# Performance work log

Hardware: AMD Instinct MI355X
Metric: run time of the kernel (lower is better)

The kernel has to match this reference:

```python
import jax, jax.numpy as jnp
import numpy as np

N = 100_000   # total nodes (batched graph)
E = 1_600_000 # edges (avg degree 16)
W = 100       # window_size (node feature dim)
H = 60        # hidden = ceil(0.6 * window_size)


def setup_inputs() -> dict:
    key = jax.random.key(0)
    ks = jax.random.split(key, 6)
    x = jax.random.normal(ks[0], (N, W), dtype=jnp.float32)
    batch_edge_index = jax.random.randint(ks[1], (2, E), 0, N, dtype=jnp.int32)
    gcn_w = jax.random.normal(ks[2], (W, W), dtype=jnp.float32) * 0.1
    gcn_b = jnp.zeros((W,), dtype=jnp.float32)
    w1 = jax.random.normal(ks[3], (H, W), dtype=jnp.float32) * 0.1
    b1 = jnp.zeros((H,), dtype=jnp.float32)
    w2 = jax.random.normal(ks[4], (W, H), dtype=jnp.float32) * 0.1
    b2 = jnp.zeros((W,), dtype=jnp.float32)
    return {"x": x, "batch_edge_index": batch_edge_index,
            "gcn_w": gcn_w, "gcn_b": gcn_b,
            "w1": w1, "b1": b1, "w2": w2, "b2": b2}


def reference(x, batch_edge_index, gcn_w, gcn_b, w1, b1, w2, b2):
    n = x.shape[0]
    # GCNConv: add self-loops, symmetric normalization D^-1/2 A D^-1/2
    loop = jnp.arange(n, dtype=batch_edge_index.dtype)
    src = jnp.concatenate([batch_edge_index[0], loop])
    dst = jnp.concatenate([batch_edge_index[1], loop])
    deg = jax.ops.segment_sum(jnp.ones(src.shape[0], jnp.float32), dst, num_segments=n)
    dinv = jnp.where(deg > 0, jax.lax.rsqrt(deg), 0.0)
    norm = dinv[src] * dinv[dst]                      # [E+N]
    xw = x @ gcn_w.T                                  # [N, W] linear transform
    msg = xw[src] * norm[:, None]                     # gather + scale
    out = jax.ops.segment_sum(msg, dst, num_segments=n) + gcn_b  # scatter-add
    # relu + tanh MLP head
    h = jax.nn.relu(out)
    h = jnp.tanh(h @ w1.T + b1)
    return jnp.tanh(h @ w2.T + b2)
```

## Files before the change

kernel.cpp:

```cpp
#include <hip/hip_runtime.h>
#include <hip/hip_bf16.h>

#define WDIM 100
#define HDIM 60
#define NPART 8
#define CAP 64

typedef short bf16x8 __attribute__((ext_vector_type(8)));
typedef float f32x4 __attribute__((ext_vector_type(4)));

__device__ inline unsigned short bf_hi_u(float v) {
    return __bfloat16_as_ushort(__float2bfloat16(v));
}
__device__ inline unsigned int pack2(float v0, float v1) {
    return (unsigned int)bf_hi_u(v0) | ((unsigned int)bf_hi_u(v1) << 16);
}
__device__ inline float fast_tanh(float x) {
    float xc = fminf(fmaxf(x, -15.f), 15.f);
    float t = __expf(2.f * xc);
    return __fdividef(t - 1.f, t + 1.f);
}

__global__ __launch_bounds__(256) void k_zero(int* __restrict__ cnt, int N) {
    int i = blockIdx.x * blockDim.x + threadIdx.x;
    int stride = gridDim.x * blockDim.x;
    for (int idx = i; idx < N; idx += stride) cnt[idx] = 0;
}

__global__ __launch_bounds__(256) void k_fill(const int* __restrict__ src,
                                              const int* __restrict__ dst,
                                              int* __restrict__ cursor,
                                              int* __restrict__ e_idx, int E, int npp) {
    const int xcd = blockIdx.x & (NPART - 1);
    const int lo = xcd * npp, hi = lo + npp;
    const int4* __restrict__ dst4 = (const int4*)dst;
    const int4* __restrict__ src4 = (const int4*)src;
    int E4 = E >> 2;
    int i = (blockIdx.x >> 3) * blockDim.x + threadIdx.x;
    int stride = (gridDim.x >> 3) * blockDim.x;
    for (int e = i; e < E4; e += stride) {
        int4 d = dst4[e];
        int4 s = src4[e];
        if (d.x >= lo && d.x < hi) {
            int p = atomicAdd(&cursor[d.x], 1);
            if (p < CAP) e_idx[(size_t)d.x * CAP + p] = s.x;
        }
        if (d.y >= lo && d.y < hi) {
            int p = atomicAdd(&cursor[d.y], 1);
            if (p < CAP) e_idx[(size_t)d.y * CAP + p] = s.y;
        }
        if (d.z >= lo && d.z < hi) {
            int p = atomicAdd(&cursor[d.z], 1);
            if (p < CAP) e_idx[(size_t)d.z * CAP + p] = s.z;
        }
        if (d.w >= lo && d.w < hi) {
            int p = atomicAdd(&cursor[d.w], 1);
            if (p < CAP) e_idx[(size_t)d.w * CAP + p] = s.w;
        }
    }
    if (i == 0) {
        for (int e = E4 << 2; e < E; ++e) {
            int d = dst[e];
            if (d >= lo && d < hi) {
                int p = atomicAdd(&cursor[d], 1);
                if (p < CAP) e_idx[(size_t)d * CAP + p] = src[e];
            }
        }
    }
}

__global__ __launch_bounds__(256) void k_xw(const float* __restrict__ x,
                                            const float* __restrict__ gw,
                                            const int* __restrict__ cnt,
                                            unsigned int* __restrict__ xwh,
                                            int N, int ntiles) {
    __shared__ char wlds[112 * 256];
    const int tid = threadIdx.x;
    for (int w = tid; w < 112 * 64; w += 256) {
        int j = w >> 6, kp = w & 63;
        unsigned int val = 0;
        if (j < 100 && kp < 50)
            val = pack2(gw[j * 100 + 2 * kp], gw[j * 100 + 2 * kp + 1]);
        *(unsigned int*)&wlds[j * 256 + ((kp * 4) ^ ((j & 7) << 4))] = val;
    }
    __syncthreads();

    const int wv = tid >> 6, l = tid & 63;
    const int arow = wv * 16 + (l & 15);
    const int koff = (l >> 4) * 8;
    const int cl = l & 15;
    const int nodeb = wv * 16 + (l >> 4) * 4;

    for (int tile = blockIdx.x; tile < ntiles; tile += gridDim.x) {
        const int n0 = tile * 64;
        int ga = n0 + arow;
        int grow = (ga < N) ? ga : (N - 1);
        const float* __restrict__ xr = x + (size_t)grow * 100;
        bf16x8 ah[4];
#pragma unroll
        for (int kt = 0; kt < 4; ++kt) {
            int c0 = kt * 32 + koff;
            float4 fa = (c0 + 4 <= 100) ? *(const float4*)&xr[c0]
                                        : make_float4(0.f, 0.f, 0.f, 0.f);
            float4 fb = (c0 + 8 <= 100) ? *(const float4*)&xr[c0 + 4]
                                        : make_float4(0.f, 0.f, 0.f, 0.f);
            union { unsigned int u[4]; bf16x8 v; } uu;
            uu.u[0] = pack2(fa.x, fa.y);
            uu.u[1] = pack2(fa.z, fa.w);
            uu.u[2] = pack2(fb.x, fb.y);
            uu.u[3] = pack2(fb.z, fb.w);
            ah[kt] = uu.v;
        }
        float dir[4];
#pragma unroll
        for (int r = 0; r < 4; ++r) {
            int g = n0 + nodeb + r;
            dir[r] = (g < N) ? rsqrtf((float)(cnt[g] + 1)) : 0.0f;
        }
#pragma unroll
        for (int jt = 0; jt < 7; ++jt) {
            f32x4 acc = {0.f, 0.f, 0.f, 0.f};
#pragma unroll
            for (int kt = 0; kt < 4; ++kt) {
                int brow = jt * 16 + cl;
                int off = brow * 256 + (((kt * 32 + koff) * 2) ^ ((brow & 7) << 4));
                bf16x8 b = *(const bf16x8*)&wlds[off];
                acc = __builtin_amdgcn_mfma_f32_16x16x32_bf16(ah[kt], b, acc, 0, 0, 0);
            }
            int col = jt * 16 + cl;
#pragma unroll
            for (int r = 0; r < 4; ++r) {
                int g = n0 + nodeb + r;
                float v = acc[r] * dir[r];
                float o = __shfl_xor(v, 1);
                if (!(cl & 1) && col < 100 && g < N)
                    xwh[(size_t)g * 50 + (col >> 1)] = pack2(v, o);
            }
        }
    }
}

__global__ __launch_bounds__(256) void k_gather(const int* __restrict__ e_idx,
                                                const int* __restrict__ cnt,
                                                const unsigned int* __restrict__ xwh,
                                                const float* __restrict__ gb,
                                                unsigned int* __restrict__ acch, int N) {
    int wid = (blockIdx.x * blockDim.x + threadIdx.x) >> 6;
    int lane = threadIdx.x & 63;
    if (wid >= N) return;
    int lanec = (lane < 50) ? lane : 0;
    const int* __restrict__ row = e_idx + (size_t)wid * CAP;
    int numraw = cnt[wid];
    int num = (numraw < CAP) ? numraw : CAP;
    float di = rsqrtf((float)(numraw + 1));
    float a0 = 0.f, a1 = 0.f, b0 = 0.f, b1 = 0.f;
    float c0 = 0.f, c1 = 0.f, d0 = 0.f, d1 = 0.f;
    float e0 = 0.f, e1 = 0.f, f0 = 0.f, f1 = 0.f;
    float g0 = 0.f, g1 = 0.f, h0 = 0.f, h1 = 0.f;
    int k = 0;
    int nn8 = num & ~7;
    if (nn8) {
        unsigned int u0 = xwh[(size_t)row[0] * 50 + lanec];
        unsigned int u1 = xwh[(size_t)row[1] * 50 + lanec];
        unsigned int u2 = xwh[(size_t)row[2] * 50 + lanec];
        unsigned int u3 = xwh[(size_t)row[3] * 50 + lanec];
        unsigned int u4 = xwh[(size_t)row[4] * 50 + lanec];
        unsigned int u5 = xwh[(size_t)row[5] * 50 + lanec];
        unsigned int u6 = xwh[(size_t)row[6] * 50 + lanec];
        unsigned int u7 = xwh[(size_t)row[7] * 50 + lanec];
        for (k = 8; k < nn8; k += 8) {
            unsigned int v0 = xwh[(size_t)row[k + 0] * 50 + lanec];
            unsigned int v1 = xwh[(size_t)row[k + 1] * 50 + lanec];
            unsigned int v2 = xwh[(size_t)row[k + 2] * 50 + lanec];
            unsigned int v3 = xwh[(size_t)row[k + 3] * 50 + lanec];
            unsigned int v4 = xwh[(size_t)row[k + 4] * 50 + lanec];
            unsigned int v5 = xwh[(size_t)row[k + 5] * 50 + lanec];
            unsigned int v6 = xwh[(size_t)row[k + 6] * 50 + lanec];
            unsigned int v7 = xwh[(size_t)row[k + 7] * 50 + lanec];
            a0 += __uint_as_float(u0 << 16); a1 += __uint_as_float(u0 & 0xffff0000u);
            b0 += __uint_as_float(u1 << 16); b1 += __uint_as_float(u1 & 0xffff0000u);
            c0 += __uint_as_float(u2 << 16); c1 += __uint_as_float(u2 & 0xffff0000u);
            d0 += __uint_as_float(u3 << 16); d1 += __uint_as_float(u3 & 0xffff0000u);
            e0 += __uint_as_float(u4 << 16); e1 += __uint_as_float(u4 & 0xffff0000u);
            f0 += __uint_as_float(u5 << 16); f1 += __uint_as_float(u5 & 0xffff0000u);
            g0 += __uint_as_float(u6 << 16); g1 += __uint_as_float(u6 & 0xffff0000u);
            h0 += __uint_as_float(u7 << 16); h1 += __uint_as_float(u7 & 0xffff0000u);
            u0 = v0; u1 = v1; u2 = v2; u3 = v3;
            u4 = v4; u5 = v5; u6 = v6; u7 = v7;
        }
        a0 += __uint_as_float(u0 << 16); a1 += __uint_as_float(u0 & 0xffff0000u);
        b0 += __uint_as_float(u1 << 16); b1 += __uint_as_float(u1 & 0xffff0000u);
        c0 += __uint_as_float(u2 << 16); c1 += __uint_as_float(u2 & 0xffff0000u);
        d0 += __uint_as_float(u3 << 16); d1 += __uint_as_float(u3 & 0xffff0000u);
        e0 += __uint_as_float(u4 << 16); e1 += __uint_as_float(u4 & 0xffff0000u);
        f0 += __uint_as_float(u5 << 16); f1 += __uint_as_float(u5 & 0xffff0000u);
        g0 += __uint_as_float(u6 << 16); g1 += __uint_as_float(u6 & 0xffff0000u);
        h0 += __uint_as_float(u7 << 16); h1 += __uint_as_float(u7 & 0xffff0000u);
        k = nn8;
    }
    for (; k < num; ++k) {
        unsigned int u = xwh[(size_t)row[k] * 50 + lanec];
        a0 += __uint_as_float(u << 16); a1 += __uint_as_float(u & 0xffff0000u);
    }
    unsigned int us = xwh[(size_t)wid * 50 + lanec];
    float s0 = ((a0 + b0) + (c0 + d0)) + ((e0 + f0) + (g0 + h0)) + __uint_as_float(us << 16);
    float s1 = ((a1 + b1) + (c1 + d1)) + ((e1 + f1) + (g1 + h1)) + __uint_as_float(us & 0xffff0000u);
    if (lane < 50) {
        float2 gbv = *(const float2*)(gb + 2 * lane);
        float v0 = fmaxf(fmaf(s0, di, gbv.x), 0.0f);
        float v1 = fmaxf(fmaf(s1, di, gbv.y), 0.0f);
        acch[(size_t)wid * 50 + lane] = pack2(v0, v1);
    }
}

__global__ __launch_bounds__(256) void k_hout(const unsigned int* __restrict__ acch,
                                              const float* __restrict__ w1,
                                              const float* __restrict__ b1,
                                              const float* __restrict__ w2,
                                              const float* __restrict__ b2,
                                              float* __restrict__ out,
                                              int N, int ntiles) {
    __shared__ char w1lds[64 * 256];
    __shared__ char w2lds[112 * 128];
    __shared__ char hlds[64 * 128];
    const int tid = threadIdx.x;

    for (int w = tid; w < 64 * 64; w += 256) {
        int j = w >> 6, kp = w & 63;
        unsigned int val = 0;
        if (j < 60 && kp < 50)
            val = pack2(w1[j * 100 + 2 * kp], w1[j * 100 + 2 * kp + 1]);
        *(unsigned int*)&w1lds[j * 256 + ((kp * 4) ^ ((j & 7) << 4))] = val;
    }
    for (int w = tid; w < 112 * 32; w += 256) {
        int j = w >> 5, kp = w & 31;
        unsigned int val = 0;
        if (j < 100 && kp < 30)
            val = pack2(w2[j * 60 + 2 * kp], w2[j * 60 + 2 * kp + 1]);
        *(unsigned int*)&w2lds[j * 128 + ((kp * 4) ^ ((j & 7) << 4))] = val;
    }
    __syncthreads();

    const int wv = tid >> 6, l = tid & 63;
    const int arow = wv * 16 + (l & 15);
    const int koff = (l >> 4) * 8;
    const int cl = l & 15;
    const int nodeb = wv * 16 + (l >> 4) * 4;

    for (int tile = blockIdx.x; tile < ntiles; tile += gridDim.x) {
        const int n0 = tile * 64;
        int ga = n0 + arow;
        int grow = (ga < N) ? ga : (N - 1);
        const unsigned int* __restrict__ ar = acch + (size_t)grow * 50;
        bf16x8 ah2[4];
#pragma unroll
        for (int kt = 0; kt < 4; ++kt) {
            int c0 = kt * 32 + koff;
            int w0 = c0 >> 1;
            uint4 u = make_uint4(0u, 0u, 0u, 0u);
            if (c0 + 8 <= 100) {
                u = *(const uint4*)&ar[w0];
            } else if (c0 + 4 <= 100) {
                uint2 t = *(const uint2*)&ar[w0];
                u.x = t.x; u.y = t.y;
            }
            union { uint4 q; bf16x8 v; } uu; uu.q = u;
            ah2[kt] = uu.v;
        }
        __syncthreads();

#pragma unroll
        for (int jt = 0; jt < 4; ++jt) {
            f32x4 acc = {0.f, 0.f, 0.f, 0.f};
#pragma unroll
            for (int kt = 0; kt < 4; ++kt) {
                int brow = jt * 16 + cl;
                int off = brow * 256 + (((kt * 32 + koff) * 2) ^ ((brow & 7) << 4));
                bf16x8 b = *(const bf16x8*)&w1lds[off];
                acc = __builtin_amdgcn_mfma_f32_16x16x32_bf16(ah2[kt], b, acc, 0, 0, 0);
            }
            int col = jt * 16 + cl;
            float bias = (col < 60) ? b1[col] : 0.0f;
#pragma unroll
            for (int r = 0; r < 4; ++r) {
                float hv = (col < 60) ? fast_tanh(acc[r] + bias) : 0.0f;
                int node = nodeb + r;
                *(unsigned short*)&hlds[node * 128 + ((col * 2) ^ ((node & 7) << 4))] = bf_hi_u(hv);
            }
        }
        __syncthreads();

        bf16x8 ah3[2];
#pragma unroll
        for (int kt = 0; kt < 2; ++kt) {
            int off = arow * 128 + (((kt * 32 + koff) * 2) ^ ((arow & 7) << 4));
            ah3[kt] = *(const bf16x8*)&hlds[off];
        }

#pragma unroll
        for (int jt = 0; jt < 7; ++jt) {
            f32x4 acc = {0.f, 0.f, 0.f, 0.f};
#pragma unroll
            for (int kt = 0; kt < 2; ++kt) {
                int brow = jt * 16 + cl;
                int off = brow * 128 + (((kt * 32 + koff) * 2) ^ ((brow & 7) << 4));
                bf16x8 b = *(const bf16x8*)&w2lds[off];
                acc = __builtin_amdgcn_mfma_f32_16x16x32_bf16(ah3[kt], b, acc, 0, 0, 0);
            }
            int col = jt * 16 + cl;
            float bias = (col < 100) ? b2[col] : 0.0f;
#pragma unroll
            for (int r = 0; r < 4; ++r) {
                int g = n0 + nodeb + r;
                if (g < N && col < 100)
                    out[(size_t)g * 100 + col] = fast_tanh(acc[r] + bias);
            }
        }
    }
}

extern "C" void kernel_launch(void* const* d_in, const int* in_sizes, int n_in,
                              void* d_out, int out_size, void* d_ws, size_t ws_size,
                              hipStream_t stream) {
    const float* x   = (const float*)d_in[0];
    const int*   ei  = (const int*)d_in[1];
    const float* gw  = (const float*)d_in[2];
    const float* gb  = (const float*)d_in[3];
    const float* w1  = (const float*)d_in[4];
    const float* b1  = (const float*)d_in[5];
    const float* w2  = (const float*)d_in[6];
    const float* b2  = (const float*)d_in[7];
    float* out = (float*)d_out;

    const int W = in_sizes[3];
    const int N = in_sizes[0] / W;
    const int E = in_sizes[1] / 2;

    const int* src = ei;
    const int* dst = ei + E;

    unsigned int* xwh  = (unsigned int*)d_ws;
    unsigned int* acch = xwh + (size_t)N * 50;
    int*   e_idx = (int*)(acch + (size_t)N * 50);
    int*   cursor = e_idx + (size_t)N * CAP;

    const int B = 256;
    const int NT = (N + 63) / 64;
    const int npp = (N + NPART - 1) / NPART;
    auto blocks = [](long long work, int cap) {
        long long b = (work + 255) / 256;
        return (int)(b < cap ? b : cap);
    };

    k_zero<<<blocks(N, 2048), B, 0, stream>>>(cursor, N);
    k_fill<<<8192, B, 0, stream>>>(src, dst, cursor, e_idx, E, npp);
    k_xw<<<782, B, 0, stream>>>(x, gw, cursor, xwh, N, NT);
    k_gather<<<(N * 64 + B - 1) / B, B, 0, stream>>>(e_idx, cursor, xwh, gb, acch, N);
    k_hout<<<782, B, 0, stream>>>(acch, w1, b1, w2, b2, out, N, NT);
}
```

Baseline: 222.3 us.

## Fuse edge fill and XW GEMM into one launch, move source scaling to gather

Combines the CSR-style edge bucketing kernel and the x@W^T MFMA kernel into one launch: the first 4096 blocks do the atomic fill and the rest compute XW, so the two independent stages can run concurrently. To remove XW's dependence on degree counts, the source-side D^-1/2 scaling moves from XW into the gather, which now loads cnt for each neighbor and applies rsqrt per edge. This adds one extra random 4-byte load and rsqrt per edge in the gather. The fill grid also drops from 8192 to 4096 blocks.

```diff
diff --git a/kernel.cpp b/kernel.cpp
--- a/kernel.cpp
+++ b/kernel.cpp
@@ -5,6 +5,7 @@
 #define HDIM 60
 #define NPART 8
 #define CAP 64
+#define FILLB 4096
 
 typedef short bf16x8 __attribute__((ext_vector_type(8)));
 typedef float f32x4 __attribute__((ext_vector_type(4)));
@@ -27,55 +28,59 @@
     for (int idx = i; idx < N; idx += stride) cnt[idx] = 0;
 }
 
-__global__ __launch_bounds__(256) void k_fill(const int* __restrict__ src,
-                                              const int* __restrict__ dst,
-                                              int* __restrict__ cursor,
-                                              int* __restrict__ e_idx, int E, int npp) {
-    const int xcd = blockIdx.x & (NPART - 1);
-    const int lo = xcd * npp, hi = lo + npp;
-    const int4* __restrict__ dst4 = (const int4*)dst;
-    const int4* __restrict__ src4 = (const int4*)src;
-    int E4 = E >> 2;
-    int i = (blockIdx.x >> 3) * blockDim.x + threadIdx.x;
-    int stride = (gridDim.x >> 3) * blockDim.x;
-    for (int e = i; e < E4; e += stride) {
-        int4 d = dst4[e];
-        int4 s = src4[e];
-        if (d.x >= lo && d.x < hi) {
-            int p = atomicAdd(&cursor[d.x], 1);
-            if (p < CAP) e_idx[(size_t)d.x * CAP + p] = s.x;
-        }
-        if (d.y >= lo && d.y < hi) {
-            int p = atomicAdd(&cursor[d.y], 1);
-            if (p < CAP) e_idx[(size_t)d.y * CAP + p] = s.y;
-        }
-        if (d.z >= lo && d.z < hi) {
-            int p = atomicAdd(&cursor[d.z], 1);
-            if (p < CAP) e_idx[(size_t)d.z * CAP + p] = s.z;
-        }
-        if (d.w >= lo && d.w < hi) {
-            int p = atomicAdd(&cursor[d.w], 1);
-            if (p < CAP) e_idx[(size_t)d.w * CAP + p] = s.w;
-        }
-    }
-    if (i == 0) {
-        for (int e = E4 << 2; e < E; ++e) {
-            int d = dst[e];
-            if (d >= lo && d < hi) {
-                int p = atomicAdd(&cursor[d], 1);
-                if (p < CAP) e_idx[(size_t)d * CAP + p] = src[e];
-            }
-        }
-    }
-}
-
-__global__ __launch_bounds__(256) void k_xw(const float* __restrict__ x,
-                                            const float* __restrict__ gw,
-                                            const int* __restrict__ cnt,
-                                            unsigned int* __restrict__ xwh,
-                                            int N, int ntiles) {
+__global__ __launch_bounds__(256) void k_fillxw(const int* __restrict__ src,
+                                                const int* __restrict__ dst,
+                                                int* __restrict__ cursor,
+                                                int* __restrict__ e_idx,
+                                                int E, int npp,
+                                                const float* __restrict__ x,
+                                                const float* __restrict__ gw,
+                                                unsigned int* __restrict__ xwh,
+                                                int N, int ntiles) {
     __shared__ char wlds[112 * 256];
     const int tid = threadIdx.x;
+    const int b = blockIdx.x;
+
+    if (b < FILLB) {
+        const int xcd = b & (NPART - 1);
+        const int lo = xcd * npp, hi = lo + npp;
+        const int4* __restrict__ dst4 = (const int4*)dst;
+        const int4* __restrict__ src4 = (const int4*)src;
+        int E4 = E >> 2;
+        int i = (b >> 3) * 256 + tid;
+        int stride = (FILLB >> 3) * 256;
+        for (int e = i; e < E4; e += stride) {
+            int4 d = dst4[e];
+            int4 s = src4[e];
+            if (d.x >= lo && d.x < hi) {
+                int p = atomicAdd(&cursor[d.x], 1);
+                if (p < CAP) e_idx[(size_t)d.x * CAP + p] = s.x;
+            }
+            if (d.y >= lo && d.y < hi) {
+                int p = atomicAdd(&cursor[d.y], 1);
+                if (p < CAP) e_idx[(size_t)d.y * CAP + p] = s.y;
+            }
+            if (d.z >= lo && d.z < hi) {
+                int p = atomicAdd(&cursor[d.z], 1);
+                if (p < CAP) e_idx[(size_t)d.z * CAP + p] = s.z;
+            }
+            if (d.w >= lo && d.w < hi) {
+                int p = atomicAdd(&cursor[d.w], 1);
+                if (p < CAP) e_idx[(size_t)d.w * CAP + p] = s.w;
+            }
+        }
+        if (i == 0) {
+            for (int e = E4 << 2; e < E; ++e) {
+                int d = dst[e];
+                if (d >= lo && d < hi) {
+                    int p = atomicAdd(&cursor[d], 1);
+                    if (p < CAP) e_idx[(size_t)d * CAP + p] = src[e];
+                }
+            }
+        }
+        return;
+    }
+
     for (int w = tid; w < 112 * 64; w += 256) {
         int j = w >> 6, kp = w & 63;
         unsigned int val = 0;
@@ -90,8 +95,9 @@
     const int koff = (l >> 4) * 8;
     const int cl = l & 15;
     const int nodeb = wv * 16 + (l >> 4) * 4;
-
-    for (int tile = blockIdx.x; tile < ntiles; tile += gridDim.x) {
+    const int xwb = gridDim.x - FILLB;
+
+    for (int tile = b - FILLB; tile < ntiles; tile += xwb) {
         const int n0 = tile * 64;
         int ga = n0 + arow;
         int grow = (ga < N) ? ga : (N - 1);
@@ -111,12 +117,6 @@
             uu.u[3] = pack2(fb.z, fb.w);
             ah[kt] = uu.v;
         }
-        float dir[4];
-#pragma unroll
-        for (int r = 0; r < 4; ++r) {
-            int g = n0 + nodeb + r;
-            dir[r] = (g < N) ? rsqrtf((float)(cnt[g] + 1)) : 0.0f;
-        }
 #pragma unroll
         for (int jt = 0; jt < 7; ++jt) {
             f32x4 acc = {0.f, 0.f, 0.f, 0.f};
@@ -124,14 +124,14 @@
             for (int kt = 0; kt < 4; ++kt) {
                 int brow = jt * 16 + cl;
                 int off = brow * 256 + (((kt * 32 + koff) * 2) ^ ((brow & 7) << 4));
-                bf16x8 b = *(const bf16x8*)&wlds[off];
-                acc = __builtin_amdgcn_mfma_f32_16x16x32_bf16(ah[kt], b, acc, 0, 0, 0);
+                bf16x8 bb = *(const bf16x8*)&wlds[off];
+                acc = __builtin_amdgcn_mfma_f32_16x16x32_bf16(ah[kt], bb, acc, 0, 0, 0);
             }
             int col = jt * 16 + cl;
 #pragma unroll
             for (int r = 0; r < 4; ++r) {
                 int g = n0 + nodeb + r;
-                float v = acc[r] * dir[r];
+                float v = acc[r];
                 float o = __shfl_xor(v, 1);
                 if (!(cl & 1) && col < 100 && g < N)
                     xwh[(size_t)g * 50 + (col >> 1)] = pack2(v, o);
@@ -160,51 +160,74 @@
     int k = 0;
     int nn8 = num & ~7;
     if (nn8) {
-        unsigned int u0 = xwh[(size_t)row[0] * 50 + lanec];
-        unsigned int u1 = xwh[(size_t)row[1] * 50 + lanec];
-        unsigned int u2 = xwh[(size_t)row[2] * 50 + lanec];
-        unsigned int u3 = xwh[(size_t)row[3] * 50 + lanec];
-        unsigned int u4 = xwh[(size_t)row[4] * 50 + lanec];
-        unsigned int u5 = xwh[(size_t)row[5] * 50 + lanec];
-        unsigned int u6 = xwh[(size_t)row[6] * 50 + lanec];
-        unsigned int u7 = xwh[(size_t)row[7] * 50 + lanec];
+        int i0 = row[0], i1 = row[1], i2 = row[2], i3 = row[3];
+        int i4 = row[4], i5 = row[5], i6 = row[6], i7 = row[7];
+        unsigned int u0 = xwh[(size_t)i0 * 50 + lanec];
+        unsigned int u1 = xwh[(size_t)i1 * 50 + lanec];
+        unsigned int u2 = xwh[(size_t)i2 * 50 + lanec];
+        unsigned int u3 = xwh[(size_t)i3 * 50 + lanec];
+        unsigned int u4 = xwh[(size_t)i4 * 50 + lanec];
+        unsigned int u5 = xwh[(size_t)i5 * 50 + lanec];
+        unsigned int u6 = xwh[(size_t)i6 * 50 + lanec];
+        unsigned int u7 = xwh[(size_t)i7 * 50 + lanec];
+        int q0 = cnt[i0], q1 = cnt[i1], q2 = cnt[i2], q3 = cnt[i3];
+        int q4 = cnt[i4], q5 = cnt[i5], q6 = cnt[i6], q7 = cnt[i7];
         for (k = 8; k < nn8; k += 8) {
-            unsigned int v0 = xwh[(size_t)row[k + 0] * 50 + lanec];
-            unsigned int v1 = xwh[(size_t)row[k + 1] * 50 + lanec];
-            unsigned int v2 = xwh[(size_t)row[k + 2] * 50 + lanec];
-            unsigned int v3 = xwh[(size_t)row[k + 3] * 50 + lanec];
-            unsigned int v4 = xwh[(size_t)row[k + 4] * 50 + lanec];
-            unsigned int v5 = xwh[(size_t)row[k + 5] * 50 + lanec];
-            unsigned int v6 = xwh[(size_t)row[k + 6] * 50 + lanec];
-            unsigned int v7 = xwh[(size_t)row[k + 7] * 50 + lanec];
-            a0 += __uint_as_float(u0 << 16); a1 += __uint_as_float(u0 & 0xffff0000u);
-            b0 += __uint_as_float(u1 << 16); b1 += __uint_as_float(u1 & 0xffff0000u);
-            c0 += __uint_as_float(u2 << 16); c1 += __uint_as_float(u2 & 0xffff0000u);
-            d0 += __uint_as_float(u3 << 16); d1 += __uint_as_float(u3 & 0xffff0000u);
-            e0 += __uint_as_float(u4 << 16); e1 += __uint_as_float(u4 & 0xffff0000u);
-            f0 += __uint_as_float(u5 << 16); f1 += __uint_as_float(u5 & 0xffff0000u);
-            g0 += __uint_as_float(u6 << 16); g1 += __uint_as_float(u6 & 0xffff0000u);
-            h0 += __uint_as_float(u7 << 16); h1 += __uint_as_float(u7 & 0xffff0000u);
+            int j0 = row[k + 0], j1 = row[k + 1], j2 = row[k + 2], j3 = row[k + 3];
+            int j4 = row[k + 4], j5 = row[k + 5], j6 = row[k + 6], j7 = row[k + 7];
+            unsigned int v0 = xwh[(size_t)j0 * 50 + lanec];
+            unsigned int v1 = xwh[(size_t)j1 * 50 + lanec];
+            unsigned int v2 = xwh[(size_t)j2 * 50 + lanec];
+            unsigned int v3 = xwh[(size_t)j3 * 50 + lanec];
+            unsigned int v4 = xwh[(size_t)j4 * 50 + lanec];
+            unsigned int v5 = xwh[(size_t)j5 * 50 + lanec];
+            unsigned int v6 = xwh[(size_t)j6 * 50 + lanec];
+            unsigned int v7 = xwh[(size_t)j7 * 50 + lanec];
+            int p0 = cnt[j0], p1 = cnt[j1], p2 = cnt[j2], p3 = cnt[j3];
+            int p4 = cnt[j4], p5 = cnt[j5], p6 = cnt[j6], p7 = cnt[j7];
+            float r0 = rsqrtf((float)(q0 + 1)), r1 = rsqrtf((float)(q1 + 1));
+            float r2 = rsqrtf((float)(q2 + 1)), r3 = rsqrtf((float)(q3 + 1));
+            float r4 = rsqrtf((float)(q4 + 1)), r5 = rsqrtf((float)(q5 + 1));
+            float r6 = rsqrtf((float)(q6 + 1)), r7 = rsqrtf((float)(q7 + 1));
+            a0 = fmaf(__uint_as_float(u0 << 16), r0, a0); a1 = fmaf(__uint_as_float(u0 & 0xffff0000u), r0, a1);
+            b0 = fmaf(__uint_as_float(u1 << 16), r1, b0); b1 = fmaf(__uint_as_float(u1 & 0xffff0000u), r1, b1);
+            c0 = fmaf(__uint_as_float(u2 << 16), r2, c0); c1 = fmaf(__uint_as_float(u2 & 0xffff0000u), r2, c1);
+            d0 = fmaf(__uint_as_float(u3 << 16), r3, d0); d1 = fmaf(__uint_as_float(u3 & 0xffff0000u), r3, d1);
+            e0 = fmaf(__uint_as_float(u4 << 16), r4, e0); e1 = fmaf(__uint_as_float(u4 & 0xffff0000u), r4, e1);
+            f0 = fmaf(__uint_as_float(u5 << 16), r5, f0); f1 = fmaf(__uint_as_float(u5 & 0xffff0000u), r5, f1);
+            g0 = fmaf(__uint_as_float(u6 << 16), r6, g0); g1 = fmaf(__uint_as_float(u6 & 0xffff0000u), r6, g1);
+            h0 = fmaf(__uint_as_float(u7 << 16), r7, h0); h1 = fmaf(__uint_as_float(u7 & 0xffff0000u), r7, h1);
             u0 = v0; u1 = v1; u2 = v2; u3 = v3;
             u4 = v4; u5 = v5; u6 = v6; u7 = v7;
-        }
-        a0 += __uint_as_float(u0 << 16); a1 += __uint_as_float(u0 & 0xffff0000u);
-        b0 += __uint_as_float(u1 << 16); b1 += __uint_as_float(u1 & 0xffff0000u);
-        c0 += __uint_as_float(u2 << 16); c1 += __uint_as_float(u2 & 0xffff0000u);
-        d0 += __uint_as_float(u3 << 16); d1 += __uint_as_float(u3 & 0xffff0000u);
-        e0 += __uint_as_float(u4 << 16); e1 += __uint_as_float(u4 & 0xffff0000u);
-        f0 += __uint_as_float(u5 << 16); f1 += __uint_as_float(u5 & 0xffff0000u);
-        g0 += __uint_as_float(u6 << 16); g1 += __uint_as_float(u6 & 0xffff0000u);
-        h0 += __uint_as_float(u7 << 16); h1 += __uint_as_float(u7 & 0xffff0000u);
+            q0 = p0; q1 = p1; q2 = p2; q3 = p3;
+            q4 = p4; q5 = p5; q6 = p6; q7 = p7;
+        }
+        float r0 = rsqrtf((float)(q0 + 1)), r1 = rsqrtf((float)(q1 + 1));
+        float r2 = rsqrtf((float)(q2 + 1)), r3 = rsqrtf((float)(q3 + 1));
+        float r4 = rsqrtf((float)(q4 + 1)), r5 = rsqrtf((float)(q5 + 1));
+        float r6 = rsqrtf((float)(q6 + 1)), r7 = rsqrtf((float)(q7 + 1));
+        a0 = fmaf(__uint_as_float(u0 << 16), r0, a0); a1 = fmaf(__uint_as_float(u0 & 0xffff0000u), r0, a1);
+        b0 = fmaf(__uint_as_float(u1 << 16), r1, b0); b1 = fmaf(__uint_as_float(u1 & 0xffff0000u), r1, b1);
+        c0 = fmaf(__uint_as_float(u2 << 16), r2, c0); c1 = fmaf(__uint_as_float(u2 & 0xffff0000u), r2, c1);
+        d0 = fmaf(__uint_as_float(u3 << 16), r3, d0); d1 = fmaf(__uint_as_float(u3 & 0xffff0000u), r3, d1);
+        e0 = fmaf(__uint_as_float(u4 << 16), r4, e0); e1 = fmaf(__uint_as_float(u4 & 0xffff0000u), r4, e1);
+        f0 = fmaf(__uint_as_float(u5 << 16), r5, f0); f1 = fmaf(__uint_as_float(u5 & 0xffff0000u), r5, f1);
+        g0 = fmaf(__uint_as_float(u6 << 16), r6, g0); g1 = fmaf(__uint_as_float(u6 & 0xffff0000u), r6, g1);
+        h0 = fmaf(__uint_as_float(u7 << 16), r7, h0); h1 = fmaf(__uint_as_float(u7 & 0xffff0000u), r7, h1);
         k = nn8;
     }
     for (; k < num; ++k) {
-        unsigned int u = xwh[(size_t)row[k] * 50 + lanec];
-        a0 += __uint_as_float(u << 16); a1 += __uint_as_float(u & 0xffff0000u);
+        int s = row[k];
+        unsigned int u = xwh[(size_t)s * 50 + lanec];
+        float r = rsqrtf((float)(cnt[s] + 1));
+        a0 = fmaf(__uint_as_float(u << 16), r, a0);
+        a1 = fmaf(__uint_as_float(u & 0xffff0000u), r, a1);
     }
     unsigned int us = xwh[(size_t)wid * 50 + lanec];
-    float s0 = ((a0 + b0) + (c0 + d0)) + ((e0 + f0) + (g0 + h0)) + __uint_as_float(us << 16);
-    float s1 = ((a1 + b1) + (c1 + d1)) + ((e1 + f1) + (g1 + h1)) + __uint_as_float(us & 0xffff0000u);
+    float s0 = ((a0 + b0) + (c0 + d0)) + ((e0 + f0) + (g0 + h0))
+             + di * __uint_as_float(us << 16);
+    float s1 = ((a1 + b1) + (c1 + d1)) + ((e1 + f1) + (g1 + h1))
+             + di * __uint_as_float(us & 0xffff0000u);
     if (lane < 50) {
         float2 gbv = *(const float2*)(gb + 2 * lane);
         float v0 = fmaxf(fmaf(s0, di, gbv.x), 0.0f);
@@ -353,8 +376,8 @@
     };
 
     k_zero<<<blocks(N, 2048), B, 0, stream>>>(cursor, N);
-    k_fill<<<8192, B, 0, stream>>>(src, dst, cursor, e_idx, E, npp);
-    k_xw<<<782, B, 0, stream>>>(x, gw, cursor, xwh, N, NT);
+    k_fillxw<<<FILLB + 782, B, 0, stream>>>(src, dst, cursor, e_idx, E, npp,
+                                            x, gw, xwh, N, NT);
     k_gather<<<(N * 64 + B - 1) / B, B, 0, stream>>>(e_idx, cursor, xwh, gb, acch, N);
     k_hout<<<782, B, 0, stream>>>(acch, w1, b1, w2, b2, out, N, NT);
 }
```

After: 221.5 us. About the same (-0.3%).
